# Optimization experiments

Hardware: AMD Instinct MI355X
Metric: run time of the kernel (lower is better)

## Reference

```python
import jax, jax.numpy as jnp
import numpy as np
from jax import lax

B, T, D, H = 64, 512, 256, 256


def lstm_scan(x_seq, Wih, Whh, bih, bhh):
    """Run an LSTMCell over time. x_seq: [B, T, D] -> hidden states [B, T, H].
    Gate order i, f, g, o (torch LSTMCell convention)."""
    Bv, Tv, _ = x_seq.shape
    Hv = Whh.shape[1]
    # Precompute input projection once: [B, T, 4H]
    x_proj = jnp.einsum('btd,gd->btg', x_seq, Wih) + bih + bhh

    def step(carry, xp):
        h, c = carry
        gates = xp + h @ Whh.T  # [B, 4H]
        i, f, g, o = jnp.split(gates, 4, axis=-1)
        c = jax.nn.sigmoid(f) * c + jax.nn.sigmoid(i) * jnp.tanh(g)
        h = jax.nn.sigmoid(o) * jnp.tanh(c)
        return (h, c), h

    init = (jnp.zeros((Bv, Hv), x_seq.dtype), jnp.zeros((Bv, Hv), x_seq.dtype))
    _, hs = lax.scan(step, init, jnp.swapaxes(x_proj, 0, 1))  # [T, B, H]
    return jnp.swapaxes(hs, 0, 1)


def bilstm(x, input_length, Wih_f, Whh_f, bih_f, bhh_f, Wih_b, Whh_b, bih_b, bhh_b):
    Bv, L, _ = x.shape
    t = jnp.arange(L)
    lens = input_length.astype(jnp.int32)
    # Inversed input exactly as _get_inversed_input: for t < len -> x[len-1-t],
    # for t >= len -> x[L-1-(t-len)] (unused tail, faithful to original).
    inv_idx = L - 1 - ((L - lens[:, None] + t[None, :]) % L)  # [B, L]
    xn = jnp.take_along_axis(x, inv_idx[:, :, None], axis=1)

    fwd_h = lstm_scan(x, Wih_f, Whh_f, bih_f, bhh_f)   # [B, L, H]
    bwd_h = lstm_scan(xn, Wih_b, Whh_b, bih_b, bhh_b)  # [B, L, H]

    # Re-reverse the backward states over valid region; zero-pad beyond length.
    mask = t[None, :] < lens[:, None]                   # [B, L]
    bwd_idx = jnp.clip(lens[:, None] - 1 - t[None, :], 0, L - 1)
    bwd_g = jnp.take_along_axis(bwd_h, bwd_idx[:, :, None], axis=1)
    out = jnp.concatenate([fwd_h, bwd_g], axis=-1)      # [B, L, 2H]
    return jnp.where(mask[:, :, None], out, jnp.zeros((), out.dtype))


def setup_inputs() -> dict:
    key = jax.random.key(0)
    ks = jax.random.split(key, 10)
    s = 0.05
    return {
        'x': jax.random.normal(ks[0], (B, T, D), jnp.float32),
        'input_length': jax.random.randint(ks[1], (B,), 1, T + 1, jnp.int32),
        'Wih_f': jax.random.normal(ks[2], (4 * H, D), jnp.float32) * s,
        'Whh_f': jax.random.normal(ks[3], (4 * H, H), jnp.float32) * s,
        'bih_f': jax.random.normal(ks[4], (4 * H,), jnp.float32) * s,
        'bhh_f': jax.random.normal(ks[5], (4 * H,), jnp.float32) * s,
        'Wih_b': jax.random.normal(ks[6], (4 * H, D), jnp.float32) * s,
        'Whh_b': jax.random.normal(ks[7], (4 * H, H), jnp.float32) * s,
        'bih_b': jax.random.normal(ks[8], (4 * H,), jnp.float32) * s,
        'bhh_b': jax.random.normal(ks[9], (4 * H,), jnp.float32) * s,
    }


def reference(x, input_length, Wih_f, Whh_f, bih_f, bhh_f, Wih_b, Whh_b, bih_b, bhh_b):
    return bilstm(x, input_length, Wih_f, Whh_f, bih_f, bhh_f, Wih_b, Whh_b, bih_b, bhh_b)
```

## Files before the change

kernel.cpp:

```cpp
#include <hip/hip_runtime.h>
#include <cstdio>


typedef unsigned short ushort_t;
typedef __attribute__((ext_vector_type(8))) short short8;
typedef __attribute__((ext_vector_type(4))) float f32x4;
typedef __attribute__((ext_vector_type(4))) int i32x4;

__device__ __forceinline__ ushort_t f2bf(float f) {
    union { float f; unsigned u; } v; v.f = f;
    unsigned r = v.u + 0x7fffu + ((v.u >> 16) & 1u);
    return (ushort_t)(r >> 16);
}
__device__ __forceinline__ float bf2f(ushort_t h) {
    union { unsigned u; float f; } v; v.u = ((unsigned)h) << 16;
    return v.f;
}

__device__ __forceinline__ float fexp2(float x) {
#if __has_builtin(__builtin_amdgcn_exp2f)
    return __builtin_amdgcn_exp2f(x);
#else
    return exp2f(x);
#endif
}
__device__ __forceinline__ float frcp(float x) {
#if __has_builtin(__builtin_amdgcn_rcpf)
    return __builtin_amdgcn_rcpf(x);
#else
    return 1.0f / x;
#endif
}
__device__ __forceinline__ float fsig(float x) {
    return frcp(1.0f + fexp2(-1.44269504089f * x));
}
__device__ __forceinline__ float ftanh(float x) {
    float e = fexp2(2.88539008178f * x);
    return 1.0f - 2.0f * frcp(e + 1.0f);
}

__device__ __forceinline__ void lds_barrier() {
    asm volatile("s_waitcnt lgkmcnt(0)\n\ts_barrier" ::: "memory");
}

__device__ __forceinline__ void async_load16(const void* g, void* l) {
    __builtin_amdgcn_global_load_lds(
        (const __attribute__((address_space(1))) void*)g,
        (__attribute__((address_space(3))) void*)l, 16, 0, 0);
}

__global__ __launch_bounds__(256) void k_f2bf(const float* __restrict__ in,
                                              ushort_t* __restrict__ out, int n) {
    int i = (blockIdx.x * 256 + threadIdx.x) * 4;
    if (i + 3 < n) {
        float4 v = *(const float4*)&in[i];
        ushort4 o;
        o.x = f2bf(v.x); o.y = f2bf(v.y); o.z = f2bf(v.z); o.w = f2bf(v.w);
        *(ushort4*)&out[i] = o;
    }
}

__global__ __launch_bounds__(256) void k_wih(const float* __restrict__ wihf,
                                             const float* __restrict__ wihb,
                                             ushort_t* __restrict__ dst) {
    int d = blockIdx.y;
    int n = blockIdx.x * 4 + (threadIdx.x >> 6);
    int l = threadIdx.x & 63;
    const float* src = (d ? wihb : wihf) + (size_t)n * 256;
    float4 v = *(const float4*)&src[l * 4];
    int np = (n & 255) * 4 + (n >> 8);
    ushort4 o;
    o.x = f2bf(v.x); o.y = f2bf(v.y); o.z = f2bf(v.z); o.w = f2bf(v.w);
    *(ushort4*)&dst[((size_t)d * 1024 + np) * 256 + l * 4] = o;
}

__global__ __launch_bounds__(256) void k_bias(const float* __restrict__ bihf,
                                              const float* __restrict__ bhhf,
                                              const float* __restrict__ bihb,
                                              const float* __restrict__ bhhb,
                                              float* __restrict__ bv) {
    int i = blockIdx.x * 256 + threadIdx.x;
    int d = i >> 10, n = i & 1023;
    float s = d ? (bihb[n] + bhhb[n]) : (bihf[n] + bhhf[n]);
    bv[d * 1024 + (n & 255) * 4 + (n >> 8)] = s;
}

__global__ __launch_bounds__(256) void k_quant(const float* __restrict__ whhf,
                                               const float* __restrict__ whhb,
                                               int* __restrict__ wmf,
                                               float* __restrict__ fscale4) {
    int rowg = blockIdx.x * 4 + (threadIdx.x >> 6);
    int l = threadIdx.x & 63;
    int d = rowg >> 10;
    int row = rowg & 1023;
    const float* W = (d ? whhb : whhf) + (size_t)row * 256;
    float4 v = *(const float4*)&W[l * 4];
    float m = fmaxf(fmaxf(fabsf(v.x), fabsf(v.y)), fmaxf(fabsf(v.z), fabsf(v.w)));
    #pragma unroll
    for (int off = 32; off > 0; off >>= 1) m = fmaxf(m, __shfl_xor(m, off));
    float inv = (m > 0.0f) ? (127.0f / m) : 0.0f;
    int q0 = __float2int_rn(v.x * inv);
    int q1 = __float2int_rn(v.y * inv);
    int q2 = __float2int_rn(v.z * inv);
    int q3 = __float2int_rn(v.w * inv);
    q0 = min(127, max(-127, q0)); q1 = min(127, max(-127, q1));
    q2 = min(127, max(-127, q2)); q3 = min(127, max(-127, q3));
    int packed = (q0 & 255) | ((q1 & 255) << 8) | ((q2 & 255) << 16) | ((q3 & 255) << 24);
    int j = row & 255, gate = row >> 8;
    int row_p = j * 4 + gate;
    int Mt = row_p >> 4, rl = row_p & 15;
    int Kt = l >> 4, lg = (l >> 2) & 3, dw = l & 3;
    wmf[d * 65536 + ((Mt * 4 + Kt) * 64 + lg * 16 + rl) * 4 + dw] = packed;
    if (l == 0) fscale4[d * 1024 + row_p] = m / (127.0f * 127.0f);
}

#define LDSOFF(r, kc) ((r) * 32 + ((((kc) + ((r) >> 1)) & 3) * 8))

__global__ __launch_bounds__(256) void k_gemm(const ushort_t* __restrict__ A,
                                              const ushort_t* __restrict__ Bw,
                                              const float* __restrict__ biasv,
                                              ushort_t* __restrict__ Xp) {
    const int dir = blockIdx.z;
    const ushort_t* Bmat = Bw + dir * 262144;
    const float* bv = biasv + dir * 1024;
    ushort_t* C = Xp + (size_t)dir * 33554432;
    const int tn = blockIdx.x;
    const int tm = blockIdx.y;
    const int tid = threadIdx.x;
    const int w = tid >> 6, l = tid & 63;
    const int wm = w & 1, wn = w >> 1;

    __shared__ ushort_t As[128 * 32];
    __shared__ ushort_t Bs[128 * 32];

    f32x4 acc[4][4];
    #pragma unroll
    for (int i = 0; i < 4; i++)
        #pragma unroll
        for (int jj = 0; jj < 4; jj++) acc[i][jj] = (f32x4){0.f, 0.f, 0.f, 0.f};

    const int r0 = tid >> 2, cb = tid & 3;
    const int cs = (cb - (r0 >> 1)) & 3;
    const ushort_t* Arow0 = &A[(size_t)(tm * 128 + r0) * 256 + cs * 8];
    const ushort_t* Arow1 = Arow0 + (size_t)64 * 256;
    const ushort_t* Brow0 = &Bmat[(size_t)(tn * 128 + r0) * 256 + cs * 8];
    const ushort_t* Brow1 = Brow0 + (size_t)64 * 256;
    ushort_t* const ldsA0 = &As[w * 512];
    ushort_t* const ldsA1 = &As[2048 + w * 512];
    ushort_t* const ldsB0 = &Bs[w * 512];
    ushort_t* const ldsB1 = &Bs[2048 + w * 512];

    for (int kb = 0; kb < 8; kb++) {
        __syncthreads();
        async_load16(Arow0 + kb * 32, ldsA0);
        async_load16(Arow1 + kb * 32, ldsA1);
        async_load16(Brow0 + kb * 32, ldsB0);
        async_load16(Brow1 + kb * 32, ldsB1);
        asm volatile("s_waitcnt vmcnt(0)" ::: "memory");
        __syncthreads();
        short8 af[4], bfr[4];
        const int q = l >> 4;
        #pragma unroll
        for (int mt = 0; mt < 4; mt++) {
            int rr = wm * 64 + mt * 16 + (l & 15);
            af[mt] = *(const short8*)&As[LDSOFF(rr, q)];
        }
        #pragma unroll
        for (int nt = 0; nt < 4; nt++) {
            int rr = wn * 64 + nt * 16 + (l & 15);
            bfr[nt] = *(const short8*)&Bs[LDSOFF(rr, q)];
        }
        #pragma unroll
        for (int mt = 0; mt < 4; mt++)
            #pragma unroll
            for (int nt = 0; nt < 4; nt++)
                acc[mt][nt] = __builtin_amdgcn_mfma_f32_16x16x32_bf16(
                    af[mt], bfr[nt], acc[mt][nt], 0, 0, 0);
    }
    #pragma unroll
    for (int nt = 0; nt < 4; nt++) {
        int n = tn * 128 + wn * 64 + nt * 16 + (l & 15);
        float bn = bv[n];
        #pragma unroll
        for (int mt = 0; mt < 4; mt++) {
            #pragma unroll
            for (int rr = 0; rr < 4; rr++) {
                int m = tm * 128 + wm * 64 + mt * 16 + (l >> 4) * 4 + rr;
                C[(size_t)m * 1024 + n] = f2bf(acc[mt][nt][rr] + bn);
            }
        }
    }
}

__global__ __launch_bounds__(512, 2) void k_rec(const ushort_t* __restrict__ xproj,
                                                const int* __restrict__ wmf,
                                                const float* __restrict__ fscale4,
                                                const int* __restrict__ lens,
                                                float* __restrict__ out) {
    const int b = blockIdx.x, d = blockIdx.y;
    const int tid = threadIdx.x;
    const int w = tid >> 6, l = tid & 63;
    int len = lens[b];
    if (len < 1) len = 1;
    if (len > 512) len = 512;
    const int lenm1 = len - 1;
    const bool dneg = (d != 0);
    const ushort_t* xp = xproj + ((size_t)d * 64 + b) * 524288;

    const int rg = l >> 4;
    const int rg16 = rg * 16;
    const int til = l & 7;
    const bool act = (l & 15) < 8;
    const int j = (w * 8 + til) * 4 + rg;

    i32x4 wf[8][4];
    const int* wb = wmf + d * 65536;
    #pragma unroll
    for (int i = 0; i < 8; i++)
        #pragma unroll
        for (int kt = 0; kt < 4; kt++)
            wf[i][kt] = *(const i32x4*)&wb[(((w * 8 + i) * 4 + kt) * 64 + l) * 4];
    #pragma unroll
    for (int i = 0; i < 8; i++)
        #pragma unroll
        for (int kt = 0; kt < 4; kt++)
            asm volatile("" : "+v"(wf[i][kt]));

    float4 fr = *(const float4*)&fscale4[d * 1024 + 4 * j];

    __shared__ char h8[2][256] __attribute__((aligned(16)));
    if (tid < 64) ((int*)h8)[tid] = 0;

    {
        float4 z = {0.f, 0.f, 0.f, 0.f};
        int total4 = (512 - len) * 64;
        for (int i = tid; i < total4; i += 512) {
            int t = len + (i >> 6);
            int c4 = i & 63;
            *(float4*)&out[((size_t)b * 512 + t) * 512 + d * 256 + c4 * 4] = z;
        }
    }
    __syncthreads();

    float c_state = 0.0f;
    const i32x4 z4 = {0, 0, 0, 0};
    const char* const xpl = (const char*)(xp + 4 * j);
    char* const outl = (char*)(out + (size_t)b * 262144 + d * 256 + j);

    uint2 xe = *(const uint2*)(xpl + (size_t)(dneg ? lenm1 : 0) * 2048);
    uint2 xo;
    {
        int sc = (1 < lenm1) ? 1 : lenm1;
        xo = *(const uint2*)(xpl + (size_t)(dneg ? (lenm1 - sc) : sc) * 2048);
    }

#define REC_STEP(RB, WB, XREG, S)                                              \
    do {                                                                       \
        const char* hbp = (const char*)h8[RB];                                 \
        i32x4 h0 = *(const i32x4*)(hbp + rg16);                                \
        i32x4 h1 = *(const i32x4*)(hbp + 64 + rg16);                           \
        i32x4 h2 = *(const i32x4*)(hbp + 128 + rg16);                          \
        i32x4 h3 = *(const i32x4*)(hbp + 192 + rg16);                          \
        uint2 xc = XREG;                                                       \
        {                                                                      \
            int sc2 = (S) + 2; if (sc2 > lenm1) sc2 = lenm1;                   \
            int t2 = dneg ? (lenm1 - sc2) : sc2;                               \
            XREG = *(const uint2*)(xpl + (size_t)t2 * 2048);                   \
        }                                                                      \
        i32x4 acc[8];                                                          \
        _Pragma("unroll")                                                      \
        for (int i = 0; i < 8; i++)                                            \
            acc[i] = __builtin_amdgcn_mfma_i32_16x16x64_i8(wf[i][0], h0, z4, 0, 0, 0); \
        _Pragma("unroll")                                                      \
        for (int i = 0; i < 8; i++)                                            \
            acc[i] = __builtin_amdgcn_mfma_i32_16x16x64_i8(wf[i][1], h1, acc[i], 0, 0, 0); \
        _Pragma("unroll")                                                      \
        for (int i = 0; i < 8; i++)                                            \
            acc[i] = __builtin_amdgcn_mfma_i32_16x16x64_i8(wf[i][2], h2, acc[i], 0, 0, 0); \
        _Pragma("unroll")                                                      \
        for (int i = 0; i < 8; i++)                                            \
            acc[i] = __builtin_amdgcn_mfma_i32_16x16x64_i8(wf[i][3], h3, acc[i], 0, 0, 0); \
        if (act) {                                                             \
            i32x4 q0 = (til & 1) ? acc[1] : acc[0];                            \
            i32x4 q1 = (til & 1) ? acc[3] : acc[2];                            \
            i32x4 q2 = (til & 1) ? acc[5] : acc[4];                            \
            i32x4 q3 = (til & 1) ? acc[7] : acc[6];                            \
            i32x4 r0 = (til & 2) ? q1 : q0;                                    \
            i32x4 r1 = (til & 2) ? q3 : q2;                                    \
            i32x4 u  = (til & 4) ? r1 : r0;                                    \
            float pi = bf2f((ushort_t)(xc.x & 0xffffu)) + fr.x * (float)u.x;   \
            float pf = bf2f((ushort_t)(xc.x >> 16))     + fr.y * (float)u.y;   \
            float pg = bf2f((ushort_t)(xc.y & 0xffffu)) + fr.z * (float)u.z;   \
            float po = bf2f((ushort_t)(xc.y >> 16))     + fr.w * (float)u.w;   \
            float ig = fsig(pi), fg = fsig(pf), gg = ftanh(pg), og = fsig(po); \
            c_state = fg * c_state + ig * gg;                                  \
            float h = og * ftanh(c_state);                                     \
            int qq = __float2int_rn(h * 127.0f);                               \
            qq = min(127, max(-127, qq));                                      \
            h8[WB][j] = (char)qq;                                              \
            int t = dneg ? (lenm1 - (S)) : (S);                                \
            *(float*)(outl + (size_t)t * 2048) = h;                            \
        }                                                                      \
        lds_barrier();                                                         \
    } while (0)

    int s = 0;
    for (; s + 1 < len; s += 2) {
        REC_STEP(0, 1, xe, s);
        REC_STEP(1, 0, xo, s + 1);
    }
    if (len & 1) {
        REC_STEP(0, 1, xe, s);
    }
#undef REC_STEP
}

extern "C" void kernel_launch(void* const* d_in, const int* in_sizes, int n_in,
                              void* d_out, int out_size, void* d_ws, size_t ws_size,
                              hipStream_t stream) {
    (void)in_sizes; (void)n_in; (void)out_size;
    const float* x    = (const float*)d_in[0];
    const int*   lens = (const int*)d_in[1];
    const float* wihf = (const float*)d_in[2];
    const float* whhf = (const float*)d_in[3];
    const float* bihf = (const float*)d_in[4];
    const float* bhhf = (const float*)d_in[5];
    const float* wihb = (const float*)d_in[6];
    const float* whhb = (const float*)d_in[7];
    const float* bihb = (const float*)d_in[8];
    const float* bhhb = (const float*)d_in[9];
    float* out = (float*)d_out;

    char* ws = (char*)d_ws;
    ushort_t* xbf    = (ushort_t*)(ws + 0);
    ushort_t* wihbf  = (ushort_t*)(ws + 16777216);
    float*    biasv  = (float*)(ws + 17825792);
    int*      wmf    = (int*)(ws + 17833984);
    float*    fscale4= (float*)(ws + 18358272);
    ushort_t* xproj  = (ushort_t*)(ws + 18366464);
    const size_t REQ = 18366464 + 134217728ull;
    if (ws_size < REQ) {
        fprintf(stderr, "kernel_launch: ws too small: %zu < %zu\n", ws_size, REQ);
    }

    k_f2bf<<<8192, 256, 0, stream>>>(x, xbf, 8388608);
    k_wih<<<dim3(256, 2), 256, 0, stream>>>(wihf, wihb, wihbf);
    k_bias<<<8, 256, 0, stream>>>(bihf, bhhf, bihb, bhhb, biasv);
    k_quant<<<512, 256, 0, stream>>>(whhf, whhb, wmf, fscale4);
    k_gemm<<<dim3(8, 256, 2), 256, 0, stream>>>(xbf, wihbf, biasv, xproj);
    k_rec<<<dim3(64, 2), 512, 0, stream>>>(xproj, wmf, fscale4, lens, out);
}
```

Baseline: 539.7 us.

## Double-buffer input-projection GEMM and skip tiles beyond sequence length

The input-projection GEMM now uses two LDS buffers, so the async global loads for k-block kb+2 are issued while k-block kb is being computed, with counted vmcnt waits. It also returns early for 128-row M tiles whose time offset lies past that batch's length, since those projections are never read by the recurrence. The cost is twice the LDS per block. The skip assumes k_rec never reads xproj rows at or beyond len in either direction.

```diff
diff --git a/kernel.cpp b/kernel.cpp
--- a/kernel.cpp
+++ b/kernel.cpp
@@ -119,19 +119,27 @@
 __global__ __launch_bounds__(256) void k_gemm(const ushort_t* __restrict__ A,
                                               const ushort_t* __restrict__ Bw,
                                               const float* __restrict__ biasv,
+                                              const int* __restrict__ lens,
                                               ushort_t* __restrict__ Xp) {
     const int dir = blockIdx.z;
+    const int tn = blockIdx.x;
+    const int tm = blockIdx.y;
+
+    {
+        int lenb = lens[tm >> 2];
+        if (lenb > 512) lenb = 512;
+        if ((tm & 3) * 128 >= lenb) return;
+    }
+
     const ushort_t* Bmat = Bw + dir * 262144;
     const float* bv = biasv + dir * 1024;
     ushort_t* C = Xp + (size_t)dir * 33554432;
-    const int tn = blockIdx.x;
-    const int tm = blockIdx.y;
     const int tid = threadIdx.x;
     const int w = tid >> 6, l = tid & 63;
     const int wm = w & 1, wn = w >> 1;
 
-    __shared__ ushort_t As[128 * 32];
-    __shared__ ushort_t Bs[128 * 32];
+    __shared__ ushort_t As[2][4096] __attribute__((aligned(16)));
+    __shared__ ushort_t Bs[2][4096] __attribute__((aligned(16)));
 
     f32x4 acc[4][4];
     #pragma unroll
@@ -145,38 +153,56 @@
     const ushort_t* Arow1 = Arow0 + (size_t)64 * 256;
     const ushort_t* Brow0 = &Bmat[(size_t)(tn * 128 + r0) * 256 + cs * 8];
     const ushort_t* Brow1 = Brow0 + (size_t)64 * 256;
-    ushort_t* const ldsA0 = &As[w * 512];
-    ushort_t* const ldsA1 = &As[2048 + w * 512];
-    ushort_t* const ldsB0 = &Bs[w * 512];
-    ushort_t* const ldsB1 = &Bs[2048 + w * 512];
-
-    for (int kb = 0; kb < 8; kb++) {
-        __syncthreads();
-        async_load16(Arow0 + kb * 32, ldsA0);
-        async_load16(Arow1 + kb * 32, ldsA1);
-        async_load16(Brow0 + kb * 32, ldsB0);
-        async_load16(Brow1 + kb * 32, ldsB1);
-        asm volatile("s_waitcnt vmcnt(0)" ::: "memory");
-        __syncthreads();
-        short8 af[4], bfr[4];
-        const int q = l >> 4;
-        #pragma unroll
-        for (int mt = 0; mt < 4; mt++) {
-            int rr = wm * 64 + mt * 16 + (l & 15);
-            af[mt] = *(const short8*)&As[LDSOFF(rr, q)];
-        }
-        #pragma unroll
-        for (int nt = 0; nt < 4; nt++) {
-            int rr = wn * 64 + nt * 16 + (l & 15);
-            bfr[nt] = *(const short8*)&Bs[LDSOFF(rr, q)];
-        }
-        #pragma unroll
-        for (int mt = 0; mt < 4; mt++)
-            #pragma unroll
-            for (int nt = 0; nt < 4; nt++)
-                acc[mt][nt] = __builtin_amdgcn_mfma_f32_16x16x32_bf16(
-                    af[mt], bfr[nt], acc[mt][nt], 0, 0, 0);
-    }
+    const int lw = w * 512;
+
+#define GISSUE(KB, CUR)                                   \
+    async_load16(Arow0 + (KB) * 32, &As[CUR][lw]);        \
+    async_load16(Arow1 + (KB) * 32, &As[CUR][2048 + lw]); \
+    async_load16(Brow0 + (KB) * 32, &Bs[CUR][lw]);        \
+    async_load16(Brow1 + (KB) * 32, &Bs[CUR][2048 + lw]);
+
+#define GCOMPUTE(CUR)                                                         \
+    {                                                                         \
+        short8 af[4], bfr[4];                                                 \
+        const int q = l >> 4;                                                 \
+        _Pragma("unroll")                                                     \
+        for (int mt = 0; mt < 4; mt++) {                                      \
+            int rr = wm * 64 + mt * 16 + (l & 15);                            \
+            af[mt] = *(const short8*)&As[CUR][LDSOFF(rr, q)];                 \
+        }                                                                     \
+        _Pragma("unroll")                                                     \
+        for (int nt = 0; nt < 4; nt++) {                                      \
+            int rr = wn * 64 + nt * 16 + (l & 15);                            \
+            bfr[nt] = *(const short8*)&Bs[CUR][LDSOFF(rr, q)];                \
+        }                                                                     \
+        _Pragma("unroll")                                                     \
+        for (int mt = 0; mt < 4; mt++)                                        \
+            _Pragma("unroll")                                                 \
+            for (int nt = 0; nt < 4; nt++)                                    \
+                acc[mt][nt] = __builtin_amdgcn_mfma_f32_16x16x32_bf16(        \
+                    af[mt], bfr[nt], acc[mt][nt], 0, 0, 0);                   \
+    }
+
+#define GSTEP(KB, CUR, VML, DOISSUE)                                          \
+    asm volatile("s_waitcnt vmcnt(" VML ")\n\ts_barrier" ::: "memory");       \
+    GCOMPUTE(CUR);                                                            \
+    lds_barrier();                                                            \
+    if (DOISSUE) { GISSUE((KB) + 2, CUR) }
+
+    GISSUE(0, 0)
+    GISSUE(1, 1)
+    GSTEP(0, 0, "4", 1)
+    GSTEP(1, 1, "4", 1)
+    GSTEP(2, 0, "4", 1)
+    GSTEP(3, 1, "4", 1)
+    GSTEP(4, 0, "4", 1)
+    GSTEP(5, 1, "4", 1)
+    GSTEP(6, 0, "4", 0)
+    GSTEP(7, 1, "0", 0)
+#undef GSTEP
+#undef GCOMPUTE
+#undef GISSUE
+
     #pragma unroll
     for (int nt = 0; nt < 4; nt++) {
         int n = tn * 128 + wn * 64 + nt * 16 + (l & 15);
@@ -347,6 +373,6 @@
     k_wih<<<dim3(256, 2), 256, 0, stream>>>(wihf, wihb, wihbf);
     k_bias<<<8, 256, 0, stream>>>(bihf, bhhf, bihb, bhhb, biasv);
     k_quant<<<512, 256, 0, stream>>>(whhf, whhb, wmf, fscale4);
-    k_gemm<<<dim3(8, 256, 2), 256, 0, stream>>>(xbf, wihbf, biasv, xproj);
+    k_gemm<<<dim3(8, 256, 2), 256, 0, stream>>>(xbf, wihbf, biasv, lens, xproj);
     k_rec<<<dim3(64, 2), 512, 0, stream>>>(xproj, wmf, fscale4, lens, out);
 }
```

Result: faster. 520.0 us (-3.7%).
